# Kernel optimization log

Measured on AMD Instinct MI355X. Metric: run time of the kernel, lower is better.

The kernel has to match this reference:

```python
import jax, jax.numpy as jnp
import numpy as np

B, C_IN, C_OUT, H, W = 16, 192, 192, 128, 128
K_EXPERTS, LATENT_DIM = 8, 64


def setup_inputs() -> dict:
    key = jax.random.key(0)
    ks = jax.random.split(key, 6)
    s = lambda fan: np.float32(1.0 / np.sqrt(fan))
    return {
        "x": jax.random.normal(ks[0], (B, C_IN, H, W), jnp.float32),
        "latent": jax.random.normal(ks[1], (B, LATENT_DIM), jnp.float32),
        # DyConv2d: K expert 3x3 kernels + biases, attention FC from latent
        "expert_w": jax.random.normal(ks[2], (K_EXPERTS, C_OUT, C_IN, 3, 3), jnp.float32) * s(C_IN * 9),
        "expert_b": jnp.zeros((K_EXPERTS, C_OUT), jnp.float32),
        "attn_w": jax.random.normal(ks[3], (K_EXPERTS, LATENT_DIM), jnp.float32) * s(LATENT_DIM),
        "attn_b": jnp.zeros((K_EXPERTS,), jnp.float32),
        # static conv2 (3x3) weights
        "conv2_w": jax.random.normal(ks[4], (C_OUT, C_OUT, 3, 3), jnp.float32) * s(C_OUT * 9),
        "conv2_b": jnp.zeros((C_OUT,), jnp.float32),
    }


def _conv3x3(x, w, b):
    # x: [N,C,H,W], w: [O,I,3,3] -> [N,O,H,W]
    y = jax.lax.conv_general_dilated(
        x, w, window_strides=(1, 1), padding=((1, 1), (1, 1)),
        dimension_numbers=("NCHW", "OIHW", "NCHW"))
    return y + b[None, :, None, None]


def reference(x, latent, expert_w, expert_b, attn_w, attn_b, conv2_w, conv2_b):
    identity = x  # stride=1, in_ch==out_ch -> adaptor is None
    # ---- DyConv2d: latent -> expert attention -> per-sample kernel ----
    attn = jax.nn.softmax(latent @ attn_w.T + attn_b, axis=-1)        # [B,K]
    w_dyn = jnp.einsum("bk,koihw->boihw", attn, expert_w)            # [B,O,I,3,3]
    b_dyn = attn @ expert_b                                          # [B,O]
    # per-sample conv, vectorized over batch
    out = jax.vmap(lambda xi, wi, bi: _conv3x3(xi[None], wi, bi)[0])(x, w_dyn, b_dyn)
    out = jax.nn.silu(out)
    # ---- static conv3x3 ----
    out = _conv3x3(out, conv2_w, conv2_b)
    out = jax.nn.silu(out)
    return out + identity
```

## Files before the change

### kernel.cpp

```cpp
#include <hip/hip_runtime.h>
#include <stdint.h>
#include <stddef.h>

typedef __bf16 bf16;
typedef bf16 bf16x8 __attribute__((ext_vector_type(8)));
typedef bf16 bf16x4 __attribute__((ext_vector_type(4)));
typedef float f32x4 __attribute__((ext_vector_type(4)));

#define B_   16
#define CI   192
#define CO   192
#define H_   128
#define W_   128
#define KE   8
#define LD   64
#define KTOT 1728
#define HP   130
#define HPHP (HP*HP)
#define NPX  (H_*W_)
#define NT   54

__device__ __forceinline__ void gll16(const void* g, void* l) {
  __builtin_amdgcn_global_load_lds(
      (const __attribute__((address_space(1))) unsigned int*)g,
      (__attribute__((address_space(3))) unsigned int*)l, 16, 0, 0);
}

__device__ __forceinline__ float silu_f(float x) {
  return x / (1.f + __expf(-x));
}

__global__ void k_attn(const float* __restrict__ latent, const float* __restrict__ attn_w,
                       const float* __restrict__ attn_b, float* __restrict__ attn) {
  int t = threadIdx.x;
  int b = t >> 3, k = t & 7;
  float s = attn_b[k];
  for (int d = 0; d < LD; ++d) s += latent[b*LD + d] * attn_w[k*LD + d];
  float m = s;
  for (int off = 4; off; off >>= 1) m = fmaxf(m, __shfl_xor(m, off, 8));
  float e = __expf(s - m);
  float sum = e;
  for (int off = 4; off; off >>= 1) sum += __shfl_xor(sum, off, 8);
  attn[t] = e / sum;
}

__global__ void k_bdyn(const float* __restrict__ attn, const float* __restrict__ expert_b,
                       float* __restrict__ bdyn) {
  int j = blockIdx.x * 256 + threadIdx.x;
  if (j >= B_ * CO) return;
  int b = j / CO, o = j - b * CO;
  float s = 0.f;
  #pragma unroll
  for (int e = 0; e < KE; ++e) s += attn[b*KE + e] * expert_b[e*CO + o];
  bdyn[j] = s;
}

__global__ void k_wdyn(const float* __restrict__ expert_w, const float* __restrict__ attn,
                       bf16* __restrict__ w_re) {
  int o = blockIdx.x;
  int chunk = o >> 4, row = o & 15, c = (row >> 1) & 3;
  __shared__ float ew[KE][KTOT];
  __shared__ float al[B_][KE];
  for (int e = 0; e < KE; ++e)
    for (int j = threadIdx.x; j < KTOT; j += 256)
      ew[e][j] = expert_w[((size_t)e*CO + o)*KTOT + j];
  if (threadIdx.x < B_*KE) al[threadIdx.x >> 3][threadIdx.x & 7] = attn[threadIdx.x];
  __syncthreads();
  for (int idx = threadIdx.x; idx < B_*KTOT; idx += 256) {
    int b = idx / KTOT, k = idx - b*KTOT;
    int kt = k >> 5, ks = (k >> 3) & 3, j = k & 7;
    int r = kt / 18, t2 = kt - r*18;
    int ibb = t2 / 3, s = t2 - ibb*3;
    int i = ibb*32 + ks*8 + j;
    float acc = 0.f;
    #pragma unroll
    for (int e = 0; e < KE; ++e) acc += al[b][e] * ew[e][i*9 + r*3 + s];
    int slot = row*4 + (ks ^ c);
    w_re[((((size_t)b*NT + kt)*12 + chunk)*64 + slot)*8 + j] = (bf16)acc;
  }
}

__global__ void k_w2re(const float* __restrict__ conv2_w, bf16* __restrict__ w2_re) {
  int o = blockIdx.x;
  int chunk = o >> 4, row = o & 15, c = (row >> 1) & 3;
  __shared__ float cw[KTOT];
  for (int j = threadIdx.x; j < KTOT; j += 256) cw[j] = conv2_w[(size_t)o*KTOT + j];
  __syncthreads();
  for (int k = threadIdx.x; k < KTOT; k += 256) {
    int kt = k >> 5, ks = (k >> 3) & 3, j = k & 7;
    int r = kt / 18, t2 = kt - r*18;
    int ibb = t2 / 3, s = t2 - ibb*3;
    int i = ibb*32 + ks*8 + j;
    int slot = row*4 + (ks ^ c);
    w2_re[(((size_t)kt*12 + chunk)*64 + slot)*8 + j] = (bf16)cw[i*9 + r*3 + s];
  }
}

__global__ void k_xpack(const float* __restrict__ x, bf16* __restrict__ xpack) {
  int h2 = blockIdx.x, ib = blockIdx.y, b = blockIdx.z;
  size_t rowbase = (((size_t)b*24 + ib)*HP + h2)*HP;
  int t = threadIdx.x;
  if (h2 == 0 || h2 == HP-1) {
    uint4 z = make_uint4(0,0,0,0);
    for (int w = t; w < HP; w += 128) *(uint4*)(xpack + (rowbase + w)*8) = z;
    return;
  }
  __shared__ float tt[8][128];
  int h = h2 - 1;
  #pragma unroll
  for (int ii = 0; ii < 8; ++ii)
    tt[ii][t] = x[(((size_t)b*CI + ib*8 + ii)*H_ + h)*W_ + t];
  __syncthreads();
  bf16x8 v;
  #pragma unroll
  for (int ii = 0; ii < 8; ++ii) v[ii] = (bf16)tt[ii][t];
  *(bf16x8*)(xpack + (rowbase + t + 1)*8) = v;
  if (t == 0) {
    uint4 z = make_uint4(0,0,0,0);
    *(uint4*)(xpack + rowbase*8) = z;
    *(uint4*)(xpack + (rowbase + HP-1)*8) = z;
  }
}

__global__ void k_midborder(bf16* __restrict__ midpack) {
  int bi = blockIdx.x;
  size_t base = (size_t)bi * HPHP;
  uint4 z = make_uint4(0,0,0,0);
  for (int j = threadIdx.x; j < 516; j += 256) {
    int h2, w2;
    if (j < 130)      { h2 = 0;       w2 = j; }
    else if (j < 260) { h2 = 129;     w2 = j - 130; }
    else if (j < 388) { h2 = j - 259; w2 = 0; }
    else              { h2 = j - 387; w2 = 129; }
    *(uint4*)(midpack + (base + (size_t)h2*HP + w2)*8) = z;
  }
}

template<int MODE>
__global__ __launch_bounds__(256, 2)
void k_conv(const bf16* __restrict__ wre, const bf16* __restrict__ inpack,
            const float* __restrict__ bias_g, const bf16* __restrict__ respack,
            bf16* __restrict__ outpack, float* __restrict__ outp) {
  const int tid  = threadIdx.x;
  const int lane = tid & 63;
  const int wv   = tid >> 6;
  const int wm   = wv >> 1;
  const int wn   = wv & 1;
  const int l15  = lane & 15, l4 = lane >> 4;

  const int bid  = blockIdx.x;
  const int n    = (bid & 7) * 128 + (bid >> 3);
  const int b    = n >> 6;
  const int tile = n & 63;
  const int p0   = tile * 256;
  const int h0   = tile * 2;

  __shared__ __align__(16) bf16 Alds[3][12*512];
  __shared__ __align__(16) bf16 Blds[2][4*2560];
  __shared__ float bias_lds[CO];

  if (tid < CO) bias_lds[tid] = (MODE == 0) ? bias_g[b*CO + tid] : bias_g[tid];

  const size_t wbase = (MODE == 0) ? ((size_t)b*CO*KTOT) : 0;

  const bf16* aS = wre + wbase + (size_t)wv*512 + lane*8;
  const bf16* bbase = inpack + (((size_t)b*24 + wv)*HPHP + (size_t)h0*HP)*8 + lane*8;
  int ibm = 0; ptrdiff_t boffEl = 0;

  auto stageA = [&](bf16* dbuf) {
    bf16* d = dbuf + wv*512;
    gll16(aS,        d);
    gll16(aS + 2048, d + 2048);
    gll16(aS + 4096, d + 4096);
    aS += 6144;
  };
  auto stageB = [&](bf16* dbuf) {
    const bf16* src = bbase + boffEl;
    bf16* d = dbuf + wv*2560;
    gll16(src,        d);
    gll16(src +  512, d +  512);
    gll16(src + 1024, d + 1024);
    gll16(src + 1536, d + 1536);
    gll16(src + 1568, d + 1568);
    if (++ibm == 6) { ibm = 0; boffEl += (ptrdiff_t)(HP - 20*HPHP)*8; }
    else boffEl += (ptrdiff_t)4*HPHP*8;
  };

  f32x4 acc[6][8];
  #pragma unroll
  for (int mf = 0; mf < 6; ++mf)
    #pragma unroll
    for (int nf = 0; nf < 8; ++nf)
      #pragma unroll
      for (int jj = 0; jj < 4; ++jj) acc[mf][nf][jj] = 0.f;

  const int sw = l15*4 + (l4 ^ ((l15 >> 1) & 3));
  const int bvb = l4*2560 + (wn*130 + l15)*8;

  stageA(Alds[0]);
  stageA(Alds[1]);
  stageB(Blds[0]);

  bf16* Bcur = (bf16*)Blds[0];
  bf16* Bnxt = (bf16*)Blds[1];

  for (int m = 0; m < 18; ++m) {
    #pragma unroll
    for (int s = 0; s < 3; ++s) {
      if (s == 2) {
        if (m == 17) asm volatile("s_waitcnt vmcnt(0)" ::: "memory");
        else         asm volatile("s_waitcnt vmcnt(8)" ::: "memory");
      } else {
        asm volatile("s_waitcnt vmcnt(3)" ::: "memory");
      }
      asm volatile("s_barrier" ::: "memory");

      const bf16* A = Alds[s];
      bf16x8 af0 = *(const bf16x8*)(A + (wm*6 + 0)*512 + sw*8);
      bf16x8 af1 = *(const bf16x8*)(A + (wm*6 + 1)*512 + sw*8);
      bf16x8 af2 = *(const bf16x8*)(A + (wm*6 + 2)*512 + sw*8);
      bf16x8 af3 = *(const bf16x8*)(A + (wm*6 + 3)*512 + sw*8);
      bf16x8 af4 = *(const bf16x8*)(A + (wm*6 + 4)*512 + sw*8);
      bf16x8 af5 = *(const bf16x8*)(A + (wm*6 + 5)*512 + sw*8);

      if (3*m + s + 2 < NT) stageA(Alds[(s+2)%3]);
      if (s == 1 && m < 17) stageB(Bnxt);

      const bf16* bp = Bcur + bvb + s*8;
      __builtin_amdgcn_s_setprio(1);
      #pragma unroll
      for (int nf = 0; nf < 8; ++nf) {
        bf16x8 bv = *(const bf16x8*)(bp + nf*128);
        acc[0][nf] = __builtin_amdgcn_mfma_f32_16x16x32_bf16(af0, bv, acc[0][nf], 0, 0, 0);
        acc[1][nf] = __builtin_amdgcn_mfma_f32_16x16x32_bf16(af1, bv, acc[1][nf], 0, 0, 0);
        acc[2][nf] = __builtin_amdgcn_mfma_f32_16x16x32_bf16(af2, bv, acc[2][nf], 0, 0, 0);
        acc[3][nf] = __builtin_amdgcn_mfma_f32_16x16x32_bf16(af3, bv, acc[3][nf], 0, 0, 0);
        acc[4][nf] = __builtin_amdgcn_mfma_f32_16x16x32_bf16(af4, bv, acc[4][nf], 0, 0, 0);
        acc[5][nf] = __builtin_amdgcn_mfma_f32_16x16x32_bf16(af5, bv, acc[5][nf], 0, 0, 0);
      }
      __builtin_amdgcn_s_setprio(0);
    }
    { bf16* t = Bcur; Bcur = Bnxt; Bnxt = t; }
  }

  #pragma unroll
  for (int mf = 0; mf < 6; ++mf) {
    int ob = wm*96 + mf*16 + l4*4;
    #pragma unroll
    for (int nf = 0; nf < 8; ++nf) {
      int pl = wn*128 + nf*16 + l15;
      int p  = p0 + pl;
      f32x4 v = acc[mf][nf];
      int h = p >> 7, w = p & 127;
      size_t basep = (((size_t)b*24 + (ob >> 3))*HP + (h + 1))*HP + (w + 1);
      if (MODE == 0) {
        bf16x4 pk;
        #pragma unroll
        for (int jj = 0; jj < 4; ++jj) {
          float xv = v[jj] + bias_lds[ob + jj];
          pk[jj] = (bf16)silu_f(xv);
        }
        *(bf16x4*)(outpack + basep*8 + (ob & 7)) = pk;
      } else {
        bf16x4 rr = *(const bf16x4*)(respack + basep*8 + (ob & 7));
        #pragma unroll
        for (int jj = 0; jj < 4; ++jj) {
          float xv = silu_f(v[jj] + bias_lds[ob + jj]);
          size_t idx = ((size_t)b*CO + ob + jj)*NPX + p;
          outp[idx] = xv + (float)rr[jj];
        }
      }
    }
  }
}

extern "C" void kernel_launch(void* const* d_in, const int* in_sizes, int n_in,
                              void* d_out, int out_size, void* d_ws, size_t ws_size,
                              hipStream_t stream) {
  const float* x        = (const float*)d_in[0];
  const float* latent   = (const float*)d_in[1];
  const float* expert_w = (const float*)d_in[2];
  const float* expert_b = (const float*)d_in[3];
  const float* attn_w   = (const float*)d_in[4];
  const float* attn_b   = (const float*)d_in[5];
  const float* conv2_w  = (const float*)d_in[6];
  const float* conv2_b  = (const float*)d_in[7];
  float* outp = (float*)d_out;

  char* base = (char*)d_ws;
  size_t off = 0;
  float* attn = (float*)(base + off); off += 4096;
  float* bdyn = (float*)(base + off); off += 16384;
  bf16* w_re  = (bf16*)(base + off);  off += (size_t)B_*CO*KTOT*2;
  bf16* w2_re = (bf16*)(base + off);  off += (size_t)CO*KTOT*2;
  bf16* xpack = (bf16*)(base + off);  off += (size_t)B_*24*HPHP*8*2;
  bf16* midpack = (bf16*)(base + off); off += (size_t)B_*24*HPHP*8*2;
  (void)ws_size; (void)in_sizes; (void)n_in; (void)out_size;

  k_attn<<<dim3(1), dim3(128), 0, stream>>>(latent, attn_w, attn_b, attn);
  k_bdyn<<<dim3(12), dim3(256), 0, stream>>>(attn, expert_b, bdyn);
  k_wdyn<<<dim3(CO), dim3(256), 0, stream>>>(expert_w, attn, w_re);
  k_w2re<<<dim3(CO), dim3(256), 0, stream>>>(conv2_w, w2_re);
  k_xpack<<<dim3(130, 24, 16), dim3(128), 0, stream>>>(x, xpack);
  k_midborder<<<dim3(B_*24), dim3(256), 0, stream>>>(midpack);
  k_conv<0><<<dim3(1024), dim3(256), 0, stream>>>(w_re, xpack, bdyn, xpack, midpack, outp);
  k_conv<1><<<dim3(1024), dim3(256), 0, stream>>>(w2_re, midpack, conv2_b, xpack, midpack, outp);
}
```

Baseline: 501.4 us.

## Switch conv implicit GEMM to 32x32x16 MFMA with split-phase LDS loads

Replaces the 16x16x32 bf16 MFMA tiling (6x8 fragments per wave) with 32x32x16 MFMA tiles (3x4 fragments), which changes the A/B fragment addressing and the epilogue mapping. Each k-step is split into two half-K phases with extra barriers, interleaving LDS fragment loads and global-to-LDS staging with MFMA issue. Larger MFMA tiles cut LDS read traffic per flop and instruction count. The added barriers and the changed register pressure from the 16-wide accumulators could hurt occupancy or overlap.

```diff
diff --git a/kernel.cpp b/kernel.cpp
--- a/kernel.cpp
+++ b/kernel.cpp
@@ -6,6 +6,7 @@
 typedef bf16 bf16x8 __attribute__((ext_vector_type(8)));
 typedef bf16 bf16x4 __attribute__((ext_vector_type(4)));
 typedef float f32x4 __attribute__((ext_vector_type(4)));
+typedef float f32x16 __attribute__((ext_vector_type(16)));
 
 #define B_   16
 #define CI   192
@@ -146,7 +147,9 @@
   const int wv   = tid >> 6;
   const int wm   = wv >> 1;
   const int wn   = wv & 1;
-  const int l15  = lane & 15, l4 = lane >> 4;
+  const int l15  = lane & 15;
+  const int l31  = lane & 31;
+  const int lhi  = lane >> 5;
 
   const int bid  = blockIdx.x;
   const int n    = (bid & 7) * 128 + (bid >> 3);
@@ -186,20 +189,25 @@
     else boffEl += (ptrdiff_t)4*HPHP*8;
   };
 
-  f32x4 acc[6][8];
-  #pragma unroll
-  for (int mf = 0; mf < 6; ++mf)
+  f32x16 acc[3][4];
+  #pragma unroll
+  for (int mt = 0; mt < 3; ++mt)
     #pragma unroll
-    for (int nf = 0; nf < 8; ++nf)
+    for (int nt = 0; nt < 4; ++nt)
       #pragma unroll
-      for (int jj = 0; jj < 4; ++jj) acc[mf][nf][jj] = 0.f;
-
-  const int sw = l15*4 + (l4 ^ ((l15 >> 1) & 3));
-  const int bvb = l4*2560 + (wn*130 + l15)*8;
-
+      for (int jj = 0; jj < 16; ++jj) acc[mt][nt][jj] = 0.f;
+
+  const int arow   = l15;
+  const int aswz   = (arow >> 1) & 3;
+  const int achnk  = (lane >> 4) & 1;
+  const int aoff0  = arow*32 + ((lhi       ^ aswz) * 8);
+  const int aoff1  = arow*32 + (((2 + lhi) ^ aswz) * 8);
+  const int bcol   = (wn*130 + l31) * 8;
+  const int bkg    = lhi * 2560;
+
+  stageB(Blds[0]);
   stageA(Alds[0]);
   stageA(Alds[1]);
-  stageB(Blds[0]);
 
   bf16* Bcur = (bf16*)Blds[0];
   bf16* Bnxt = (bf16*)Blds[1];
@@ -213,61 +221,92 @@
       } else {
         asm volatile("s_waitcnt vmcnt(3)" ::: "memory");
       }
-      asm volatile("s_barrier" ::: "memory");
-
-      const bf16* A = Alds[s];
-      bf16x8 af0 = *(const bf16x8*)(A + (wm*6 + 0)*512 + sw*8);
-      bf16x8 af1 = *(const bf16x8*)(A + (wm*6 + 1)*512 + sw*8);
-      bf16x8 af2 = *(const bf16x8*)(A + (wm*6 + 2)*512 + sw*8);
-      bf16x8 af3 = *(const bf16x8*)(A + (wm*6 + 3)*512 + sw*8);
-      bf16x8 af4 = *(const bf16x8*)(A + (wm*6 + 4)*512 + sw*8);
-      bf16x8 af5 = *(const bf16x8*)(A + (wm*6 + 5)*512 + sw*8);
+      __builtin_amdgcn_s_barrier();
+
+      const bf16* A  = Alds[s];
+      const bf16* bp = Bcur + bkg + bcol + s*8;
+
+      bf16x8 a0 = *(const bf16x8*)(A + (wm*6 + 0 + achnk)*512 + aoff0);
+      bf16x8 a1 = *(const bf16x8*)(A + (wm*6 + 2 + achnk)*512 + aoff0);
+      bf16x8 a2 = *(const bf16x8*)(A + (wm*6 + 4 + achnk)*512 + aoff0);
+      bf16x8 b0 = *(const bf16x8*)(bp);
+      bf16x8 b1 = *(const bf16x8*)(bp + 256);
+      bf16x8 b2 = *(const bf16x8*)(bp + 512);
+      bf16x8 b3 = *(const bf16x8*)(bp + 768);
 
       if (3*m + s + 2 < NT) stageA(Alds[(s+2)%3]);
+
+      __builtin_amdgcn_s_barrier();
+      __builtin_amdgcn_s_setprio(1);
+      acc[0][0] = __builtin_amdgcn_mfma_f32_32x32x16_bf16(a0, b0, acc[0][0], 0, 0, 0);
+      acc[0][1] = __builtin_amdgcn_mfma_f32_32x32x16_bf16(a0, b1, acc[0][1], 0, 0, 0);
+      acc[0][2] = __builtin_amdgcn_mfma_f32_32x32x16_bf16(a0, b2, acc[0][2], 0, 0, 0);
+      acc[0][3] = __builtin_amdgcn_mfma_f32_32x32x16_bf16(a0, b3, acc[0][3], 0, 0, 0);
+      acc[1][0] = __builtin_amdgcn_mfma_f32_32x32x16_bf16(a1, b0, acc[1][0], 0, 0, 0);
+      acc[1][1] = __builtin_amdgcn_mfma_f32_32x32x16_bf16(a1, b1, acc[1][1], 0, 0, 0);
+      acc[1][2] = __builtin_amdgcn_mfma_f32_32x32x16_bf16(a1, b2, acc[1][2], 0, 0, 0);
+      acc[1][3] = __builtin_amdgcn_mfma_f32_32x32x16_bf16(a1, b3, acc[1][3], 0, 0, 0);
+      acc[2][0] = __builtin_amdgcn_mfma_f32_32x32x16_bf16(a2, b0, acc[2][0], 0, 0, 0);
+      acc[2][1] = __builtin_amdgcn_mfma_f32_32x32x16_bf16(a2, b1, acc[2][1], 0, 0, 0);
+      acc[2][2] = __builtin_amdgcn_mfma_f32_32x32x16_bf16(a2, b2, acc[2][2], 0, 0, 0);
+      acc[2][3] = __builtin_amdgcn_mfma_f32_32x32x16_bf16(a2, b3, acc[2][3], 0, 0, 0);
+      __builtin_amdgcn_s_setprio(0);
+
+      bf16x8 a3 = *(const bf16x8*)(A + (wm*6 + 0 + achnk)*512 + aoff1);
+      bf16x8 a4 = *(const bf16x8*)(A + (wm*6 + 2 + achnk)*512 + aoff1);
+      bf16x8 a5 = *(const bf16x8*)(A + (wm*6 + 4 + achnk)*512 + aoff1);
+      bf16x8 b4 = *(const bf16x8*)(bp + 2*2560);
+      bf16x8 b5 = *(const bf16x8*)(bp + 2*2560 + 256);
+      bf16x8 b6 = *(const bf16x8*)(bp + 2*2560 + 512);
+      bf16x8 b7 = *(const bf16x8*)(bp + 2*2560 + 768);
+
       if (s == 1 && m < 17) stageB(Bnxt);
 
-      const bf16* bp = Bcur + bvb + s*8;
+      __builtin_amdgcn_s_barrier();
       __builtin_amdgcn_s_setprio(1);
-      #pragma unroll
-      for (int nf = 0; nf < 8; ++nf) {
-        bf16x8 bv = *(const bf16x8*)(bp + nf*128);
-        acc[0][nf] = __builtin_amdgcn_mfma_f32_16x16x32_bf16(af0, bv, acc[0][nf], 0, 0, 0);
-        acc[1][nf] = __builtin_amdgcn_mfma_f32_16x16x32_bf16(af1, bv, acc[1][nf], 0, 0, 0);
-        acc[2][nf] = __builtin_amdgcn_mfma_f32_16x16x32_bf16(af2, bv, acc[2][nf], 0, 0, 0);
-        acc[3][nf] = __builtin_amdgcn_mfma_f32_16x16x32_bf16(af3, bv, acc[3][nf], 0, 0, 0);
-        acc[4][nf] = __builtin_amdgcn_mfma_f32_16x16x32_bf16(af4, bv, acc[4][nf], 0, 0, 0);
-        acc[5][nf] = __builtin_amdgcn_mfma_f32_16x16x32_bf16(af5, bv, acc[5][nf], 0, 0, 0);
-      }
+      acc[0][0] = __builtin_amdgcn_mfma_f32_32x32x16_bf16(a3, b4, acc[0][0], 0, 0, 0);
+      acc[0][1] = __builtin_amdgcn_mfma_f32_32x32x16_bf16(a3, b5, acc[0][1], 0, 0, 0);
+      acc[0][2] = __builtin_amdgcn_mfma_f32_32x32x16_bf16(a3, b6, acc[0][2], 0, 0, 0);
+      acc[0][3] = __builtin_amdgcn_mfma_f32_32x32x16_bf16(a3, b7, acc[0][3], 0, 0, 0);
+      acc[1][0] = __builtin_amdgcn_mfma_f32_32x32x16_bf16(a4, b4, acc[1][0], 0, 0, 0);
+      acc[1][1] = __builtin_amdgcn_mfma_f32_32x32x16_bf16(a4, b5, acc[1][1], 0, 0, 0);
+      acc[1][2] = __builtin_amdgcn_mfma_f32_32x32x16_bf16(a4, b6, acc[1][2], 0, 0, 0);
+      acc[1][3] = __builtin_amdgcn_mfma_f32_32x32x16_bf16(a4, b7, acc[1][3], 0, 0, 0);
+      acc[2][0] = __builtin_amdgcn_mfma_f32_32x32x16_bf16(a5, b4, acc[2][0], 0, 0, 0);
+      acc[2][1] = __builtin_amdgcn_mfma_f32_32x32x16_bf16(a5, b5, acc[2][1], 0, 0, 0);
+      acc[2][2] = __builtin_amdgcn_mfma_f32_32x32x16_bf16(a5, b6, acc[2][2], 0, 0, 0);
+      acc[2][3] = __builtin_amdgcn_mfma_f32_32x32x16_bf16(a5, b7, acc[2][3], 0, 0, 0);
       __builtin_amdgcn_s_setprio(0);
     }
     { bf16* t = Bcur; Bcur = Bnxt; Bnxt = t; }
   }
 
   #pragma unroll
-  for (int mf = 0; mf < 6; ++mf) {
-    int ob = wm*96 + mf*16 + l4*4;
+  for (int mt = 0; mt < 3; ++mt) {
     #pragma unroll
-    for (int nf = 0; nf < 8; ++nf) {
-      int pl = wn*128 + nf*16 + l15;
-      int p  = p0 + pl;
-      f32x4 v = acc[mf][nf];
-      int h = p >> 7, w = p & 127;
-      size_t basep = (((size_t)b*24 + (ob >> 3))*HP + (h + 1))*HP + (w + 1);
-      if (MODE == 0) {
-        bf16x4 pk;
-        #pragma unroll
-        for (int jj = 0; jj < 4; ++jj) {
-          float xv = v[jj] + bias_lds[ob + jj];
-          pk[jj] = (bf16)silu_f(xv);
-        }
-        *(bf16x4*)(outpack + basep*8 + (ob & 7)) = pk;
-      } else {
-        bf16x4 rr = *(const bf16x4*)(respack + basep*8 + (ob & 7));
-        #pragma unroll
-        for (int jj = 0; jj < 4; ++jj) {
-          float xv = silu_f(v[jj] + bias_lds[ob + jj]);
-          size_t idx = ((size_t)b*CO + ob + jj)*NPX + p;
-          outp[idx] = xv + (float)rr[jj];
+    for (int nt = 0; nt < 4; ++nt) {
+      int w = nt*32 + l31;
+      int p = p0 + wn*128 + w;
+      #pragma unroll
+      for (int rq = 0; rq < 4; ++rq) {
+        int ob = wm*96 + mt*32 + rq*8 + 4*lhi;
+        size_t basep = (((size_t)b*24 + (ob >> 3))*HP + (h0 + wn + 1))*HP + (w + 1);
+        if (MODE == 0) {
+          bf16x4 pk;
+          #pragma unroll
+          for (int jj = 0; jj < 4; ++jj) {
+            float xv = acc[mt][nt][rq*4 + jj] + bias_lds[ob + jj];
+            pk[jj] = (bf16)silu_f(xv);
+          }
+          *(bf16x4*)(outpack + basep*8 + (ob & 7)) = pk;
+        } else {
+          bf16x4 rr = *(const bf16x4*)(respack + basep*8 + (ob & 7));
+          #pragma unroll
+          for (int jj = 0; jj < 4; ++jj) {
+            float xv = silu_f(acc[mt][nt][rq*4 + jj] + bias_lds[ob + jj]);
+            size_t idx = ((size_t)b*CO + ob + jj)*NPX + p;
+            outp[idx] = xv + (float)rr[jj];
+          }
         }
       }
     }
```

Result: faster. 483.1 us (-3.7%).
